# Kernel optimization log

Measured on AMD Instinct MI355X. Metric: run time of the kernel, lower is better.

The kernel has to match this reference:

```python
import jax, jax.numpy as jnp
import numpy as np

N = 100000
E = 1600000
DIN = 128
DOUT = 128
NUM_STEPS = 3


def setup_inputs() -> dict:
    key = jax.random.key(0)
    ks = jax.random.split(key, 12)
    stdv = 1.0 / np.sqrt(DOUT)
    xav = np.sqrt(6.0 / (2 * DOUT + DOUT))  # xavier_uniform for [DOUT, 2*DOUT]
    return {
        "input": jax.random.normal(ks[0], (N, DIN), dtype=jnp.float32),
        "edge_row": jax.random.randint(ks[1], (E,), 0, N, dtype=jnp.int32),
        "edge_col": jax.random.randint(ks[2], (E,), 0, N, dtype=jnp.int32),
        "edge_weight": jax.random.uniform(ks[3], (E,), dtype=jnp.float32),
        "weight": jax.random.uniform(ks[4], (DIN, DOUT), jnp.float32, -stdv, stdv),
        "bias": jax.random.uniform(ks[5], (DOUT,), jnp.float32, -stdv, stdv),
        "candidate_weight": jax.random.uniform(ks[6], (DOUT, DOUT), jnp.float32, -stdv, stdv),
        "ug_W": jax.random.uniform(ks[7], (DOUT, 2 * DOUT), jnp.float32, -xav, xav),
        "ug_b": jnp.zeros((DOUT,), jnp.float32),
        "rg_W": jax.random.uniform(ks[8], (DOUT, 2 * DOUT), jnp.float32, -xav, xav),
        "rg_b": jnp.zeros((DOUT,), jnp.float32),
    }


def reference(input, edge_row, edge_col, edge_weight, weight, bias,
              candidate_weight, ug_W, ug_b, rg_W, rg_b):
    n = input.shape[0]
    # h = input @ W + b
    h = input @ weight + bias
    for _ in range(NUM_STEPS):
        # spmm: m[dst] += w_e * h[src]
        msg = edge_weight[:, None] * h[edge_col]          # [E, DOUT]
        m = jax.ops.segment_sum(msg, edge_row, num_segments=n)  # [N, DOUT]
        g = jnp.concatenate([h, m], axis=1)               # [N, 2*DOUT]
        z = jax.nn.sigmoid(g @ ug_W.T + ug_b)
        r = jax.nn.sigmoid(g @ rg_W.T + rg_b)
        cand = jnp.tanh((r * h) @ candidate_weight)
        h = z * h + (1.0 - z) * cand
    return h
```

## Files before the change

kernel.cpp:

```cpp
#include <hip/hip_runtime.h>
#include <math.h>

#define NN 100000
#define EE 1600000
#define D 128
#define NBK 782
#define SBLK 98
#define EPB 16384
#define EMAX 2048
#define INITB 3125

typedef __attribute__((ext_vector_type(8))) short short8;
typedef __attribute__((ext_vector_type(4))) float floatx4;

static __device__ __forceinline__ unsigned short f2bf(float f) {
  unsigned int u = __builtin_bit_cast(unsigned int, f);
  u = (u + 0x7fff + ((u >> 16) & 1)) >> 16;
  return (unsigned short)u;
}
static __device__ __forceinline__ unsigned int pk2(float a, float b) {
  return (unsigned int)f2bf(a) | ((unsigned int)f2bf(b) << 16);
}
static __device__ __forceinline__ float bflo(unsigned int u) { return __builtin_bit_cast(float, u << 16); }
static __device__ __forceinline__ float bfhi(unsigned int u) { return __builtin_bit_cast(float, u & 0xffff0000u); }
static __device__ __forceinline__ float bf2f(unsigned short s) {
  return __builtin_bit_cast(float, (unsigned int)s << 16);
}
static __device__ __forceinline__ float sig_f(float x) { return 1.f / (1.f + __expf(-x)); }
static __device__ __forceinline__ float tanh_f(float x) {
  float e = __expf(2.f * x);
  return 1.f - 2.f / (e + 1.f);
}
static __device__ __forceinline__ void fma8(float* acc, float w, uint4 h) {
  acc[0] += w * bflo(h.x); acc[1] += w * bfhi(h.x);
  acc[2] += w * bflo(h.y); acc[3] += w * bfhi(h.y);
  acc[4] += w * bflo(h.z); acc[5] += w * bfhi(h.z);
  acc[6] += w * bflo(h.w); acc[7] += w * bfhi(h.w);
}

__global__ __launch_bounds__(1024) void countpack(const int* __restrict__ erow, int* __restrict__ cnt_pb,
                                                  const float* __restrict__ ugW, const float* __restrict__ rgW,
                                                  const float* __restrict__ CW, const float* __restrict__ W,
                                                  unsigned int* __restrict__ packZR,
                                                  unsigned int* __restrict__ packCW,
                                                  unsigned int* __restrict__ packW) {
  __shared__ int s[NBK];
  const int tid = threadIdx.x;
  if (blockIdx.x < SBLK) {
    for (int b = tid; b < NBK; b += 1024) s[b] = 0;
    __syncthreads();
    const int base = blockIdx.x * EPB;
#pragma unroll
    for (int i = 0; i < 16; ++i) {
      int idx = base + i * 1024 + tid;
      if (idx < EE) atomicAdd(&s[erow[idx] >> 7], 1);
    }
    __syncthreads();
    for (int b = tid; b < NBK; b += 1024) cnt_pb[blockIdx.x * NBK + b] = s[b];
  } else {
    int g = (blockIdx.x - SBLK) * 16 + (tid >> 6);
    int lane = tid & 63;
    if (g < 128) {
      int nt = g >> 3, ks = g & 7;
      int o = nt * 16 + (lane & 15);
      int c0 = ks * 32 + (lane >> 4) * 8;
      const float* src = (o < 128 ? ugW + (size_t)o * 256 : rgW + (size_t)(o - 128) * 256) + c0;
      float4 f0 = ((const float4*)src)[0];
      float4 f1 = ((const float4*)src)[1];
      uint4 out;
      out.x = pk2(f0.x, f0.y);
      out.y = pk2(f0.z, f0.w);
      out.z = pk2(f1.x, f1.y);
      out.w = pk2(f1.z, f1.w);
      ((uint4*)packZR)[g * 64 + lane] = out;
    } else if (g < 192) {
      const float* M = (g < 160) ? CW : W;
      unsigned int* dst = (g < 160) ? packCW : packW;
      int gg = (g < 160) ? (g - 128) : (g - 160);
      int nt = gg >> 2, ks = gg & 3;
      int n = nt * 16 + (lane & 15);
      int k0 = ks * 32 + (lane >> 4) * 8;
      unsigned short v[8];
#pragma unroll
      for (int j = 0; j < 8; ++j) v[j] = f2bf(M[(size_t)(k0 + j) * 128 + n]);
      uint4 out;
      out.x = (unsigned int)v[0] | ((unsigned int)v[1] << 16);
      out.y = (unsigned int)v[2] | ((unsigned int)v[3] << 16);
      out.z = (unsigned int)v[4] | ((unsigned int)v[5] << 16);
      out.w = (unsigned int)v[6] | ((unsigned int)v[7] << 16);
      ((uint4*)dst)[gg * 64 + lane] = out;
    }
  }
}

__global__ __launch_bounds__(1024) void b_off(const int* __restrict__ cnt_pb,
                                              int* __restrict__ bucket_off, int* __restrict__ bucket_cur) {
  __shared__ int s[1024];
  const int t = threadIdx.x;
  int v = 0;
  if (t < NBK) {
    for (int j = 0; j < SBLK; ++j) v += cnt_pb[j * NBK + t];
  }
  s[t] = v;
  __syncthreads();
  for (int d = 1; d < 1024; d <<= 1) {
    int x = (t >= d) ? s[t - d] : 0;
    __syncthreads();
    s[t] += x;
    __syncthreads();
  }
  int excl = s[t] - v;
  if (t < NBK) { bucket_off[t] = excl; bucket_cur[t] = excl; }
  if (t == NBK - 1) bucket_off[NBK] = excl + v;
}

__global__ __launch_bounds__(1024) void b_scatter(const int* __restrict__ erow, const int* __restrict__ ecol,
                                                  const float* __restrict__ ew, const int* __restrict__ cnt_pb,
                                                  int* __restrict__ bucket_cur, int2* __restrict__ arena) {
  __shared__ int cur[NBK];
  const int tid = threadIdx.x;
  for (int b = tid; b < NBK; b += 1024) {
    int c = cnt_pb[blockIdx.x * NBK + b];
    cur[b] = c ? atomicAdd(&bucket_cur[b], c) : 0;
  }
  __syncthreads();
  const int base = blockIdx.x * EPB;
#pragma unroll
  for (int i = 0; i < 16; ++i) {
    int idx = base + i * 1024 + tid;
    if (idx < EE) {
      int r = erow[idx];
      int pos = atomicAdd(&cur[r >> 7], 1);
      int2 v;
      v.x = ecol[idx] | ((r & 127) << 24);
      v.y = __builtin_bit_cast(int, ew[idx]);
      arena[pos] = v;
    }
  }
}

__global__ __launch_bounds__(256) void sortinit(
    const int* __restrict__ bucket_off, const int2* __restrict__ arena,
    int2* __restrict__ edata, int* __restrict__ row_start,
    const float* __restrict__ X, const short* __restrict__ packW, const float* __restrict__ bias,
    unsigned short* __restrict__ h_bf) {
  __shared__ __align__(16) char smem[32 * 136 * 2];
  const int tid = threadIdx.x;

  if (blockIdx.x < NBK) {
    int* rcnt = (int*)smem;
    int* rcur = (int*)(smem + 512);
    const int b = blockIdx.x;
    const int lo = bucket_off[b], hi = bucket_off[b + 1];

    if (tid < 128) rcnt[tid] = 0;
    __syncthreads();
    for (int i = lo + tid; i < hi; i += 256) atomicAdd(&rcnt[(arena[i].x >> 24) & 127], 1);
    __syncthreads();
    int myc = (tid < 128) ? rcnt[tid] : 0;
    for (int d = 1; d < 128; d <<= 1) {
      int v = (tid < 128 && tid >= d) ? rcnt[tid - d] : 0;
      __syncthreads();
      if (tid < 128) rcnt[tid] += v;
      __syncthreads();
    }
    if (tid < 128) {
      int excl = rcnt[tid] - myc;
      rcur[tid] = lo + excl;
      int gr = b * 128 + tid;
      if (gr < NN) row_start[gr] = lo + excl;
    }
    if (b == NBK - 1 && tid == 0) row_start[NN] = hi;
    __syncthreads();

    for (int i = lo + tid; i < hi; i += 256) {
      int2 v = arena[i];
      int rl = (v.x >> 24) & 127;
      int pos = atomicAdd(&rcur[rl], 1);
      int2 o;
      o.x = v.x & 0x00FFFFFF;
      o.y = v.y;
      edata[pos] = o;
    }
  } else {
    short* sX = (short*)smem;
    const int row0 = (blockIdx.x - NBK) * 32;

    {
      int r = tid >> 3, ch = tid & 7;
      const float4* px = (const float4*)(X + (size_t)(row0 + r) * D + ch * 16);
      float4 f0 = px[0], f1 = px[1], f2 = px[2], f3 = px[3];
      uint4 o0, o1;
      o0.x = pk2(f0.x, f0.y); o0.y = pk2(f0.z, f0.w);
      o0.z = pk2(f1.x, f1.y); o0.w = pk2(f1.z, f1.w);
      o1.x = pk2(f2.x, f2.y); o1.y = pk2(f2.z, f2.w);
      o1.z = pk2(f3.x, f3.y); o1.w = pk2(f3.z, f3.w);
      *(uint4*)(sX + r * 136 + ch * 16) = o0;
      *(uint4*)(sX + r * 136 + ch * 16 + 8) = o1;
    }
    __syncthreads();

    const int wave = tid >> 6, lane = tid & 63;
    const int quad = lane >> 4, l15 = lane & 15;
    const int mh = wave & 1, nh = wave >> 1;
    const int mrow = mh * 16 + l15;

    floatx4 acc[4];
    const floatx4 zero4 = {0.f, 0.f, 0.f, 0.f};
#pragma unroll
    for (int t = 0; t < 4; ++t) acc[t] = zero4;

    const short8* pW = (const short8*)packW;
#pragma unroll
    for (int ks = 0; ks < 4; ++ks) {
      short8 a = *(const short8*)(sX + mrow * 136 + ks * 32 + quad * 8);
#pragma unroll
      for (int t = 0; t < 4; ++t) {
        short8 b = pW[((nh * 4 + t) * 4 + ks) * 64 + lane];
        acc[t] = __builtin_amdgcn_mfma_f32_16x16x32_bf16(a, b, acc[t], 0, 0, 0);
      }
    }

    __syncthreads();
#pragma unroll
    for (int t = 0; t < 4; ++t) {
      int col = nh * 64 + t * 16 + l15;
      float bv = bias[col];
#pragma unroll
      for (int reg = 0; reg < 4; ++reg) {
        int row = mh * 16 + quad * 4 + reg;
        sX[row * 136 + col] = (short)f2bf(acc[t][reg] + bv);
      }
    }
    __syncthreads();
    for (int idx = tid; idx < 512; idx += 256) {
      int r = idx >> 4, ch = idx & 15;
      *(uint4*)(h_bf + (size_t)(row0 + r) * D + ch * 8) = *(uint4*)(sX + r * 136 + ch * 8);
    }
  }
}

__global__ __launch_bounds__(512, 8) void fused_step(
    const int* __restrict__ row_start, const int2* __restrict__ edata,
    const uint4* __restrict__ h4,
    const short* __restrict__ packZR, const short* __restrict__ packCW,
    const float* __restrict__ ugb, const float* __restrict__ rgb,
    unsigned short* __restrict__ h_bf_out, float* __restrict__ h_f32_out, int last) {
  __shared__ __align__(16) short sA[32 * 264];
  __shared__ __align__(16) char sU[EMAX * 8];
  int2* sE = (int2*)sU;
  short* sRH = (short*)sU;

  const int tid = threadIdx.x;
  const int row0 = blockIdx.x * 32;
  const int wave = tid >> 6, lane = tid & 63;
  const int sub = lane >> 4, li = lane & 15;

  {
    int r = tid >> 4, ch = tid & 15;
    *(uint4*)(sA + r * 264 + ch * 8) = h4[(size_t)(row0 + r) * 16 + ch];
  }

  const int myrow = row0 + wave * 4 + sub;
  const int rs0 = row_start[myrow];
  const int rs1 = row_start[myrow + 1];
  const int seg_lo = row_start[row0];
  const int seg_hi = row_start[row0 + 32];

  float acc[8];
#pragma unroll
  for (int j = 0; j < 8; ++j) acc[j] = 0.f;

  for (int clo = seg_lo; clo < seg_hi; clo += EMAX) {
    const int chi = min(clo + EMAX, seg_hi);
    for (int i = clo + tid; i < chi; i += 512) sE[i - clo] = edata[i];
    __syncthreads();

    int kb = max(rs0, clo) - clo;
    int ke = min(rs1, chi) - clo;
    for (; kb + 2 <= ke; kb += 2) {
      int2 e0 = sE[kb];
      int2 e1 = sE[kb + 1];
      uint4 h0 = h4[(size_t)e0.x * 16 + li];
      uint4 h1 = h4[(size_t)e1.x * 16 + li];
      fma8(acc, __builtin_bit_cast(float, e0.y), h0);
      fma8(acc, __builtin_bit_cast(float, e1.y), h1);
    }
    if (kb < ke) {
      int2 e0 = sE[kb];
      uint4 h0 = h4[(size_t)e0.x * 16 + li];
      fma8(acc, __builtin_bit_cast(float, e0.y), h0);
    }
    __syncthreads();
  }

  {
    uint4 o;
    o.x = pk2(acc[0], acc[1]);
    o.y = pk2(acc[2], acc[3]);
    o.z = pk2(acc[4], acc[5]);
    o.w = pk2(acc[6], acc[7]);
    *(uint4*)(sA + (wave * 4 + sub) * 264 + 128 + li * 8) = o;
  }
  __syncthreads();

  const int quad = lane >> 4, l15 = lane & 15;
  const int mh = wave >> 2, nh = wave & 3;
  const int mrow = mh * 16 + l15;

  floatx4 accZ[2], accR[2];
  const floatx4 zero4 = {0.f, 0.f, 0.f, 0.f};
#pragma unroll
  for (int t = 0; t < 2; ++t) { accZ[t] = zero4; accR[t] = zero4; }

  const short8* pB = (const short8*)packZR;
#pragma unroll
  for (int ks = 0; ks < 8; ++ks) {
    short8 a = *(const short8*)(sA + mrow * 264 + ks * 32 + quad * 8);
#pragma unroll
    for (int t = 0; t < 2; ++t) {
      short8 bz = pB[((nh * 2 + t) * 8 + ks) * 64 + lane];
      accZ[t] = __builtin_amdgcn_mfma_f32_16x16x32_bf16(a, bz, accZ[t], 0, 0, 0);
      short8 br = pB[((8 + nh * 2 + t) * 8 + ks) * 64 + lane];
      accR[t] = __builtin_amdgcn_mfma_f32_16x16x32_bf16(a, br, accR[t], 0, 0, 0);
    }
  }

#pragma unroll
  for (int t = 0; t < 2; ++t) {
    int col = nh * 32 + t * 16 + l15;
    float zb = ugb[col], rb = rgb[col];
#pragma unroll
    for (int reg = 0; reg < 4; ++reg) {
      int row = mh * 16 + quad * 4 + reg;
      float z = sig_f(accZ[t][reg] + zb);
      float rr = sig_f(accR[t][reg] + rb);
      float hv = bf2f((unsigned short)sA[row * 264 + col]);
      sRH[row * 136 + col] = (short)f2bf(rr * hv);
      accZ[t][reg] = z;
    }
  }
  __syncthreads();

  floatx4 acc2[2];
#pragma unroll
  for (int t = 0; t < 2; ++t) acc2[t] = zero4;

  const short8* pC = (const short8*)packCW;
#pragma unroll
  for (int ks = 0; ks < 4; ++ks) {
    short8 a = *(const short8*)(sRH + mrow * 136 + ks * 32 + quad * 8);
#pragma unroll
    for (int t = 0; t < 2; ++t) {
      short8 b = pC[((nh * 2 + t) * 4 + ks) * 64 + lane];
      acc2[t] = __builtin_amdgcn_mfma_f32_16x16x32_bf16(a, b, acc2[t], 0, 0, 0);
    }
  }

#pragma unroll
  for (int t = 0; t < 2; ++t) {
    int col = nh * 32 + t * 16 + l15;
#pragma unroll
    for (int reg = 0; reg < 4; ++reg) {
      int row = mh * 16 + quad * 4 + reg;
      float cand = tanh_f(acc2[t][reg]);
      float z = accZ[t][reg];
      float hold = bf2f((unsigned short)sA[row * 264 + col]);
      float hn = z * hold + (1.f - z) * cand;
      if (last) h_f32_out[(size_t)(row0 + row) * D + col] = hn;
      else sA[row * 264 + col] = (short)f2bf(hn);
    }
  }
  if (!last) {
    __syncthreads();
    int r = tid >> 4, ch = tid & 15;
    *(uint4*)(h_bf_out + (size_t)(row0 + r) * D + ch * 8) = *(uint4*)(sA + r * 264 + ch * 8);
  }
}

extern "C" void kernel_launch(void* const* d_in, const int* in_sizes, int n_in,
                              void* d_out, int out_size, void* d_ws, size_t ws_size,
                              hipStream_t stream) {
  const float* input = (const float*)d_in[0];
  const int* erow    = (const int*)d_in[1];
  const int* ecol    = (const int*)d_in[2];
  const float* ew    = (const float*)d_in[3];
  const float* W     = (const float*)d_in[4];
  const float* bias  = (const float*)d_in[5];
  const float* CW    = (const float*)d_in[6];
  const float* ugW   = (const float*)d_in[7];
  const float* ugb   = (const float*)d_in[8];
  const float* rgW   = (const float*)d_in[9];
  const float* rgb   = (const float*)d_in[10];

  float* h_out = (float*)d_out;

  char* ws = (char*)d_ws;
  unsigned short* hA = (unsigned short*)ws;   ws += (size_t)NN * D * 2;
  unsigned short* hB = (unsigned short*)ws;   ws += (size_t)NN * D * 2;
  unsigned int* packZR = (unsigned int*)ws;   ws += 16 * 8 * 64 * 16;
  unsigned int* packCW = (unsigned int*)ws;   ws += 8 * 4 * 64 * 16;
  unsigned int* packW  = (unsigned int*)ws;   ws += 8 * 4 * 64 * 16;
  int2* arena    = (int2*)ws;                 ws += (size_t)EE * sizeof(int2);
  int2* edata    = (int2*)ws;                 ws += (size_t)EE * sizeof(int2);
  int* cnt_pb    = (int*)ws;                  ws += (size_t)SBLK * NBK * sizeof(int);
  int* bucket_off= (int*)ws;                  ws += (NBK + 1) * sizeof(int);
  int* bucket_cur= (int*)ws;                  ws += NBK * sizeof(int);
  int* row_start = (int*)ws;                  ws += (NN + 1) * sizeof(int);

  countpack<<<SBLK + 12, 1024, 0, stream>>>(erow, cnt_pb, ugW, rgW, CW, W, packZR, packCW, packW);
  b_off<<<1, 1024, 0, stream>>>(cnt_pb, bucket_off, bucket_cur);
  b_scatter<<<SBLK, 1024, 0, stream>>>(erow, ecol, ew, cnt_pb, bucket_cur, arena);
  sortinit<<<NBK + INITB, 256, 0, stream>>>(bucket_off, arena, edata, row_start,
                                            input, (const short*)packW, bias, hA);

  fused_step<<<NN / 32, 512, 0, stream>>>(row_start, edata, (const uint4*)hA,
                                          (const short*)packZR, (const short*)packCW,
                                          ugb, rgb, hB, h_out, 0);
  fused_step<<<NN / 32, 512, 0, stream>>>(row_start, edata, (const uint4*)hB,
                                          (const short*)packZR, (const short*)packCW,
                                          ugb, rgb, hA, h_out, 0);
  fused_step<<<NN / 32, 512, 0, stream>>>(row_start, edata, (const uint4*)hA,
                                          (const short*)packZR, (const short*)packCW,
                                          ugb, rgb, hB, h_out, 1);
}
```

Baseline: 490.6 us.

## Replace global CSR sort with fixed-capacity row buckets sorted in-kernel

```diff
diff --git a/kernel.cpp b/kernel.cpp
--- a/kernel.cpp
+++ b/kernel.cpp
@@ -4,11 +4,10 @@
 #define NN 100000
 #define EE 1600000
 #define D 128
-#define NBK 782
+#define NBK 3125
 #define SBLK 98
 #define EPB 16384
-#define EMAX 2048
-#define INITB 3125
+#define CAP 1024
 
 typedef __attribute__((ext_vector_type(8))) short short8;
 typedef __attribute__((ext_vector_type(4))) float floatx4;
@@ -38,25 +37,43 @@
   acc[6] += w * bflo(h.w); acc[7] += w * bfhi(h.w);
 }
 
-__global__ __launch_bounds__(1024) void countpack(const int* __restrict__ erow, int* __restrict__ cnt_pb,
-                                                  const float* __restrict__ ugW, const float* __restrict__ rgW,
-                                                  const float* __restrict__ CW, const float* __restrict__ W,
-                                                  unsigned int* __restrict__ packZR,
-                                                  unsigned int* __restrict__ packCW,
-                                                  unsigned int* __restrict__ packW) {
-  __shared__ int s[NBK];
+__global__ __launch_bounds__(1024) void scatterpack(
+    const int* __restrict__ erow, const int* __restrict__ ecol, const float* __restrict__ ew,
+    int* __restrict__ bucket_len, int2* __restrict__ arena,
+    const float* __restrict__ ugW, const float* __restrict__ rgW,
+    const float* __restrict__ CW, const float* __restrict__ W,
+    unsigned int* __restrict__ packZR, unsigned int* __restrict__ packCW,
+    unsigned int* __restrict__ packW) {
+  __shared__ int cur[NBK];
   const int tid = threadIdx.x;
   if (blockIdx.x < SBLK) {
-    for (int b = tid; b < NBK; b += 1024) s[b] = 0;
+    for (int b = tid; b < NBK; b += 1024) cur[b] = 0;
     __syncthreads();
     const int base = blockIdx.x * EPB;
+    int r[16];
 #pragma unroll
     for (int i = 0; i < 16; ++i) {
       int idx = base + i * 1024 + tid;
-      if (idx < EE) atomicAdd(&s[erow[idx] >> 7], 1);
+      r[i] = (idx < EE) ? erow[idx] : -1;
+      if (r[i] >= 0) atomicAdd(&cur[r[i] >> 5], 1);
     }
     __syncthreads();
-    for (int b = tid; b < NBK; b += 1024) cnt_pb[blockIdx.x * NBK + b] = s[b];
+    for (int b = tid; b < NBK; b += 1024) {
+      int c = cur[b];
+      cur[b] = c ? (b * CAP + atomicAdd(&bucket_len[b], c)) : 0;
+    }
+    __syncthreads();
+#pragma unroll
+    for (int i = 0; i < 16; ++i) {
+      if (r[i] >= 0) {
+        int idx = base + i * 1024 + tid;
+        int pos = atomicAdd(&cur[r[i] >> 5], 1);
+        int2 v;
+        v.x = ecol[idx] | ((r[i] & 31) << 24);
+        v.y = __builtin_bit_cast(int, ew[idx]);
+        arena[pos] = v;
+      }
+    }
   } else {
     int g = (blockIdx.x - SBLK) * 16 + (tid >> 6);
     int lane = tid & 63;
@@ -93,166 +110,84 @@
   }
 }
 
-__global__ __launch_bounds__(1024) void b_off(const int* __restrict__ cnt_pb,
-                                              int* __restrict__ bucket_off, int* __restrict__ bucket_cur) {
-  __shared__ int s[1024];
-  const int t = threadIdx.x;
-  int v = 0;
-  if (t < NBK) {
-    for (int j = 0; j < SBLK; ++j) v += cnt_pb[j * NBK + t];
-  }
-  s[t] = v;
-  __syncthreads();
-  for (int d = 1; d < 1024; d <<= 1) {
-    int x = (t >= d) ? s[t - d] : 0;
-    __syncthreads();
-    s[t] += x;
-    __syncthreads();
-  }
-  int excl = s[t] - v;
-  if (t < NBK) { bucket_off[t] = excl; bucket_cur[t] = excl; }
-  if (t == NBK - 1) bucket_off[NBK] = excl + v;
-}
-
-__global__ __launch_bounds__(1024) void b_scatter(const int* __restrict__ erow, const int* __restrict__ ecol,
-                                                  const float* __restrict__ ew, const int* __restrict__ cnt_pb,
-                                                  int* __restrict__ bucket_cur, int2* __restrict__ arena) {
-  __shared__ int cur[NBK];
-  const int tid = threadIdx.x;
-  for (int b = tid; b < NBK; b += 1024) {
-    int c = cnt_pb[blockIdx.x * NBK + b];
-    cur[b] = c ? atomicAdd(&bucket_cur[b], c) : 0;
-  }
-  __syncthreads();
-  const int base = blockIdx.x * EPB;
-#pragma unroll
-  for (int i = 0; i < 16; ++i) {
-    int idx = base + i * 1024 + tid;
-    if (idx < EE) {
-      int r = erow[idx];
-      int pos = atomicAdd(&cur[r >> 7], 1);
-      int2 v;
-      v.x = ecol[idx] | ((r & 127) << 24);
-      v.y = __builtin_bit_cast(int, ew[idx]);
-      arena[pos] = v;
-    }
-  }
-}
-
-__global__ __launch_bounds__(256) void sortinit(
-    const int* __restrict__ bucket_off, const int2* __restrict__ arena,
-    int2* __restrict__ edata, int* __restrict__ row_start,
+__global__ __launch_bounds__(256) void init_mfma(
     const float* __restrict__ X, const short* __restrict__ packW, const float* __restrict__ bias,
     unsigned short* __restrict__ h_bf) {
-  __shared__ __align__(16) char smem[32 * 136 * 2];
+  __shared__ __align__(16) short sX[32 * 136];
   const int tid = threadIdx.x;
-
-  if (blockIdx.x < NBK) {
-    int* rcnt = (int*)smem;
-    int* rcur = (int*)(smem + 512);
-    const int b = blockIdx.x;
-    const int lo = bucket_off[b], hi = bucket_off[b + 1];
-
-    if (tid < 128) rcnt[tid] = 0;
-    __syncthreads();
-    for (int i = lo + tid; i < hi; i += 256) atomicAdd(&rcnt[(arena[i].x >> 24) & 127], 1);
-    __syncthreads();
-    int myc = (tid < 128) ? rcnt[tid] : 0;
-    for (int d = 1; d < 128; d <<= 1) {
-      int v = (tid < 128 && tid >= d) ? rcnt[tid - d] : 0;
-      __syncthreads();
-      if (tid < 128) rcnt[tid] += v;
-      __syncthreads();
-    }
-    if (tid < 128) {
-      int excl = rcnt[tid] - myc;
-      rcur[tid] = lo + excl;
-      int gr = b * 128 + tid;
-      if (gr < NN) row_start[gr] = lo + excl;
-    }
-    if (b == NBK - 1 && tid == 0) row_start[NN] = hi;
-    __syncthreads();
-
-    for (int i = lo + tid; i < hi; i += 256) {
-      int2 v = arena[i];
-      int rl = (v.x >> 24) & 127;
-      int pos = atomicAdd(&rcur[rl], 1);
-      int2 o;
-      o.x = v.x & 0x00FFFFFF;
-      o.y = v.y;
-      edata[pos] = o;
-    }
-  } else {
-    short* sX = (short*)smem;
-    const int row0 = (blockIdx.x - NBK) * 32;
-
-    {
-      int r = tid >> 3, ch = tid & 7;
-      const float4* px = (const float4*)(X + (size_t)(row0 + r) * D + ch * 16);
-      float4 f0 = px[0], f1 = px[1], f2 = px[2], f3 = px[3];
-      uint4 o0, o1;
-      o0.x = pk2(f0.x, f0.y); o0.y = pk2(f0.z, f0.w);
-      o0.z = pk2(f1.x, f1.y); o0.w = pk2(f1.z, f1.w);
-      o1.x = pk2(f2.x, f2.y); o1.y = pk2(f2.z, f2.w);
-      o1.z = pk2(f3.x, f3.y); o1.w = pk2(f3.z, f3.w);
-      *(uint4*)(sX + r * 136 + ch * 16) = o0;
-      *(uint4*)(sX + r * 136 + ch * 16 + 8) = o1;
-    }
-    __syncthreads();
-
-    const int wave = tid >> 6, lane = tid & 63;
-    const int quad = lane >> 4, l15 = lane & 15;
-    const int mh = wave & 1, nh = wave >> 1;
-    const int mrow = mh * 16 + l15;
-
-    floatx4 acc[4];
-    const floatx4 zero4 = {0.f, 0.f, 0.f, 0.f};
-#pragma unroll
-    for (int t = 0; t < 4; ++t) acc[t] = zero4;
-
-    const short8* pW = (const short8*)packW;
-#pragma unroll
-    for (int ks = 0; ks < 4; ++ks) {
-      short8 a = *(const short8*)(sX + mrow * 136 + ks * 32 + quad * 8);
-#pragma unroll
-      for (int t = 0; t < 4; ++t) {
-        short8 b = pW[((nh * 4 + t) * 4 + ks) * 64 + lane];
-        acc[t] = __builtin_amdgcn_mfma_f32_16x16x32_bf16(a, b, acc[t], 0, 0, 0);
-      }
-    }
-
-    __syncthreads();
+  const int row0 = blockIdx.x * 32;
+
+  {
+    int r = tid >> 3, ch = tid & 7;
+    const float4* px = (const float4*)(X + (size_t)(row0 + r) * D + ch * 16);
+    float4 f0 = px[0], f1 = px[1], f2 = px[2], f3 = px[3];
+    uint4 o0, o1;
+    o0.x = pk2(f0.x, f0.y); o0.y = pk2(f0.z, f0.w);
+    o0.z = pk2(f1.x, f1.y); o0.w = pk2(f1.z, f1.w);
+    o1.x = pk2(f2.x, f2.y); o1.y = pk2(f2.z, f2.w);
+    o1.z = pk2(f3.x, f3.y); o1.w = pk2(f3.z, f3.w);
+    *(uint4*)(sX + r * 136 + ch * 16) = o0;
+    *(uint4*)(sX + r * 136 + ch * 16 + 8) = o1;
+  }
+  __syncthreads();
+
+  const int wave = tid >> 6, lane = tid & 63;
+  const int quad = lane >> 4, l15 = lane & 15;
+  const int mh = wave & 1, nh = wave >> 1;
+  const int mrow = mh * 16 + l15;
+
+  floatx4 acc[4];
+  const floatx4 zero4 = {0.f, 0.f, 0.f, 0.f};
+#pragma unroll
+  for (int t = 0; t < 4; ++t) acc[t] = zero4;
+
+  const short8* pW = (const short8*)packW;
+#pragma unroll
+  for (int ks = 0; ks < 4; ++ks) {
+    short8 a = *(const short8*)(sX + mrow * 136 + ks * 32 + quad * 8);
 #pragma unroll
     for (int t = 0; t < 4; ++t) {
-      int col = nh * 64 + t * 16 + l15;
-      float bv = bias[col];
-#pragma unroll
-      for (int reg = 0; reg < 4; ++reg) {
-        int row = mh * 16 + quad * 4 + reg;
-        sX[row * 136 + col] = (short)f2bf(acc[t][reg] + bv);
-      }
-    }
-    __syncthreads();
-    for (int idx = tid; idx < 512; idx += 256) {
-      int r = idx >> 4, ch = idx & 15;
-      *(uint4*)(h_bf + (size_t)(row0 + r) * D + ch * 8) = *(uint4*)(sX + r * 136 + ch * 8);
-    }
+      short8 b = pW[((nh * 4 + t) * 4 + ks) * 64 + lane];
+      acc[t] = __builtin_amdgcn_mfma_f32_16x16x32_bf16(a, b, acc[t], 0, 0, 0);
+    }
+  }
+
+  __syncthreads();
+#pragma unroll
+  for (int t = 0; t < 4; ++t) {
+    int col = nh * 64 + t * 16 + l15;
+    float bv = bias[col];
+#pragma unroll
+    for (int reg = 0; reg < 4; ++reg) {
+      int row = mh * 16 + quad * 4 + reg;
+      sX[row * 136 + col] = (short)f2bf(acc[t][reg] + bv);
+    }
+  }
+  __syncthreads();
+  for (int idx = tid; idx < 512; idx += 256) {
+    int r = idx >> 4, ch = idx & 15;
+    *(uint4*)(h_bf + (size_t)(row0 + r) * D + ch * 8) = *(uint4*)(sX + r * 136 + ch * 8);
   }
 }
 
 __global__ __launch_bounds__(512, 8) void fused_step(
-    const int* __restrict__ row_start, const int2* __restrict__ edata,
+    const int* __restrict__ bucket_len, const int2* __restrict__ arena,
     const uint4* __restrict__ h4,
     const short* __restrict__ packZR, const short* __restrict__ packCW,
     const float* __restrict__ ugb, const float* __restrict__ rgb,
     unsigned short* __restrict__ h_bf_out, float* __restrict__ h_f32_out, int last) {
   __shared__ __align__(16) short sA[32 * 264];
-  __shared__ __align__(16) char sU[EMAX * 8];
-  int2* sE = (int2*)sU;
+  __shared__ __align__(16) char sU[8704];
+  __shared__ __align__(16) int2 sE2[CAP];
+  __shared__ int rcnt[32];
+  __shared__ int rstart[32];
+  __shared__ int rcur[32];
+  int2* sE_raw = (int2*)sU;
   short* sRH = (short*)sU;
 
   const int tid = threadIdx.x;
-  const int row0 = blockIdx.x * 32;
+  const int bid = blockIdx.x;
+  const int row0 = bid * 32;
   const int wave = tid >> 6, lane = tid & 63;
   const int sub = lane >> 4, li = lane & 15;
 
@@ -261,37 +196,52 @@
     *(uint4*)(sA + r * 264 + ch * 8) = h4[(size_t)(row0 + r) * 16 + ch];
   }
 
-  const int myrow = row0 + wave * 4 + sub;
-  const int rs0 = row_start[myrow];
-  const int rs1 = row_start[myrow + 1];
-  const int seg_lo = row_start[row0];
-  const int seg_hi = row_start[row0 + 32];
-
+  const int lo = bid * CAP;
+  int len = bucket_len[bid];
+  len = (len < CAP) ? len : CAP;
+
+  if (tid < 32) rcnt[tid] = 0;
+  for (int i = tid; i < len; i += 512) sE_raw[i] = arena[lo + i];
+  __syncthreads();
+  for (int i = tid; i < len; i += 512) atomicAdd(&rcnt[(sE_raw[i].x >> 24) & 31], 1);
+  __syncthreads();
+  if (tid < 64) {
+    int v = (tid < 32) ? rcnt[tid] : 0;
+    int inc = v;
+#pragma unroll
+    for (int d = 1; d < 32; d <<= 1) {
+      int u = __shfl_up(inc, d, 64);
+      if (tid >= d) inc += u;
+    }
+    if (tid < 32) { rstart[tid] = inc - v; rcur[tid] = inc - v; }
+  }
+  __syncthreads();
+  for (int i = tid; i < len; i += 512) {
+    int2 e = sE_raw[i];
+    int pos = atomicAdd(&rcur[(e.x >> 24) & 31], 1);
+    sE2[pos] = e;
+  }
+  __syncthreads();
+
+  const int rl = wave * 4 + sub;
   float acc[8];
 #pragma unroll
   for (int j = 0; j < 8; ++j) acc[j] = 0.f;
 
-  for (int clo = seg_lo; clo < seg_hi; clo += EMAX) {
-    const int chi = min(clo + EMAX, seg_hi);
-    for (int i = clo + tid; i < chi; i += 512) sE[i - clo] = edata[i];
-    __syncthreads();
-
-    int kb = max(rs0, clo) - clo;
-    int ke = min(rs1, chi) - clo;
-    for (; kb + 2 <= ke; kb += 2) {
-      int2 e0 = sE[kb];
-      int2 e1 = sE[kb + 1];
-      uint4 h0 = h4[(size_t)e0.x * 16 + li];
-      uint4 h1 = h4[(size_t)e1.x * 16 + li];
-      fma8(acc, __builtin_bit_cast(float, e0.y), h0);
-      fma8(acc, __builtin_bit_cast(float, e1.y), h1);
-    }
-    if (kb < ke) {
-      int2 e0 = sE[kb];
-      uint4 h0 = h4[(size_t)e0.x * 16 + li];
-      fma8(acc, __builtin_bit_cast(float, e0.y), h0);
-    }
-    __syncthreads();
+  int kb = rstart[rl];
+  int ke = kb + rcnt[rl];
+  for (; kb + 2 <= ke; kb += 2) {
+    int2 e0 = sE2[kb];
+    int2 e1 = sE2[kb + 1];
+    uint4 h0 = h4[(size_t)(e0.x & 0x00FFFFFF) * 16 + li];
+    uint4 h1 = h4[(size_t)(e1.x & 0x00FFFFFF) * 16 + li];
+    fma8(acc, __builtin_bit_cast(float, e0.y), h0);
+    fma8(acc, __builtin_bit_cast(float, e1.y), h1);
+  }
+  if (kb < ke) {
+    int2 e0 = sE2[kb];
+    uint4 h0 = h4[(size_t)(e0.x & 0x00FFFFFF) * 16 + li];
+    fma8(acc, __builtin_bit_cast(float, e0.y), h0);
   }
 
   {
@@ -401,26 +351,21 @@
   unsigned int* packZR = (unsigned int*)ws;   ws += 16 * 8 * 64 * 16;
   unsigned int* packCW = (unsigned int*)ws;   ws += 8 * 4 * 64 * 16;
   unsigned int* packW  = (unsigned int*)ws;   ws += 8 * 4 * 64 * 16;
-  int2* arena    = (int2*)ws;                 ws += (size_t)EE * sizeof(int2);
-  int2* edata    = (int2*)ws;                 ws += (size_t)EE * sizeof(int2);
-  int* cnt_pb    = (int*)ws;                  ws += (size_t)SBLK * NBK * sizeof(int);
-  int* bucket_off= (int*)ws;                  ws += (NBK + 1) * sizeof(int);
-  int* bucket_cur= (int*)ws;                  ws += NBK * sizeof(int);
-  int* row_start = (int*)ws;                  ws += (NN + 1) * sizeof(int);
-
-  countpack<<<SBLK + 12, 1024, 0, stream>>>(erow, cnt_pb, ugW, rgW, CW, W, packZR, packCW, packW);
-  b_off<<<1, 1024, 0, stream>>>(cnt_pb, bucket_off, bucket_cur);
-  b_scatter<<<SBLK, 1024, 0, stream>>>(erow, ecol, ew, cnt_pb, bucket_cur, arena);
-  sortinit<<<NBK + INITB, 256, 0, stream>>>(bucket_off, arena, edata, row_start,
-                                            input, (const short*)packW, bias, hA);
-
-  fused_step<<<NN / 32, 512, 0, stream>>>(row_start, edata, (const uint4*)hA,
-                                          (const short*)packZR, (const short*)packCW,
-                                          ugb, rgb, hB, h_out, 0);
-  fused_step<<<NN / 32, 512, 0, stream>>>(row_start, edata, (const uint4*)hB,
-                                          (const short*)packZR, (const short*)packCW,
-                                          ugb, rgb, hA, h_out, 0);
-  fused_step<<<NN / 32, 512, 0, stream>>>(row_start, edata, (const uint4*)hA,
-                                          (const short*)packZR, (const short*)packCW,
-                                          ugb, rgb, hB, h_out, 1);
-}
+  int2* arena    = (int2*)ws;                 ws += (size_t)NBK * CAP * sizeof(int2);
+  int* bucket_len= (int*)ws;                  ws += NBK * sizeof(int);
+
+  hipMemsetAsync(bucket_len, 0, NBK * sizeof(int), stream);
+  scatterpack<<<SBLK + 12, 1024, 0, stream>>>(erow, ecol, ew, bucket_len, arena,
+                                              ugW, rgW, CW, W, packZR, packCW, packW);
+  init_mfma<<<NN / 32, 256, 0, stream>>>(input, (const short*)packW, bias, hA);
+
+  fused_step<<<NBK, 512, 0, stream>>>(bucket_len, arena, (const uint4*)hA,
+                                      (const short*)packZR, (const short*)packCW,
+                                      ugb, rgb, hB, h_out, 0);
+  fused_step<<<NBK, 512, 0, stream>>>(bucket_len, arena, (const uint4*)hB,
+                                      (const short*)packZR, (const short*)packCW,
+                                      ugb, rgb, hA, h_out, 0);
+  fused_step<<<NBK, 512, 0, stream>>>(bucket_len, arena, (const uint4*)hA,
+                                      (const short*)packZR, (const short*)packCW,
+                                      ugb, rgb, hB, h_out, 1);
+}
```

After: 498.6 us. About the same (+1.6%).

## Merge preprocessing kernels into one cooperative kernel with grid syncs

Applied to the files above, without the earlier changes.

```diff
diff --git a/kernel.cpp b/kernel.cpp
--- a/kernel.cpp
+++ b/kernel.cpp
@@ -1,14 +1,19 @@
 #include <hip/hip_runtime.h>
+#include <hip/hip_cooperative_groups.h>
 #include <math.h>
+
+namespace cg = cooperative_groups;
 
 #define NN 100000
 #define EE 1600000
 #define D 128
 #define NBK 782
-#define SBLK 98
-#define EPB 16384
+#define GG 256
+#define TB 1024
+#define CNTB 244
+#define EPB1 6558
+#define EPB2 6250
 #define EMAX 2048
-#define INITB 3125
 
 typedef __attribute__((ext_vector_type(8))) short short8;
 typedef __attribute__((ext_vector_type(4))) float floatx4;
@@ -38,27 +43,32 @@
   acc[6] += w * bflo(h.w); acc[7] += w * bfhi(h.w);
 }
 
-__global__ __launch_bounds__(1024) void countpack(const int* __restrict__ erow, int* __restrict__ cnt_pb,
-                                                  const float* __restrict__ ugW, const float* __restrict__ rgW,
-                                                  const float* __restrict__ CW, const float* __restrict__ W,
-                                                  unsigned int* __restrict__ packZR,
-                                                  unsigned int* __restrict__ packCW,
-                                                  unsigned int* __restrict__ packW) {
-  __shared__ int s[NBK];
+__global__ __launch_bounds__(1024) void prep(
+    const int* __restrict__ erow, const int* __restrict__ ecol, const float* __restrict__ ew,
+    const float* __restrict__ ugW, const float* __restrict__ rgW,
+    const float* __restrict__ CW, const float* __restrict__ W,
+    const float* __restrict__ X, const float* __restrict__ bias,
+    unsigned int* __restrict__ packZR, unsigned int* __restrict__ packCW,
+    unsigned int* __restrict__ packW,
+    int* __restrict__ cnt_pb, int* __restrict__ bucket_off, int* __restrict__ bucket_cur,
+    int2* __restrict__ arena, int2* __restrict__ edata, int* __restrict__ row_start,
+    unsigned short* __restrict__ h_bf) {
+  cg::grid_group grid = cg::this_grid();
+  __shared__ __align__(16) char sm[34816];
   const int tid = threadIdx.x;
-  if (blockIdx.x < SBLK) {
-    for (int b = tid; b < NBK; b += 1024) s[b] = 0;
-    __syncthreads();
-    const int base = blockIdx.x * EPB;
-#pragma unroll
-    for (int i = 0; i < 16; ++i) {
-      int idx = base + i * 1024 + tid;
-      if (idx < EE) atomicAdd(&s[erow[idx] >> 7], 1);
-    }
-    __syncthreads();
-    for (int b = tid; b < NBK; b += 1024) cnt_pb[blockIdx.x * NBK + b] = s[b];
+  const int blk = blockIdx.x;
+
+  if (blk < CNTB) {
+    int* s = (int*)sm;
+    for (int b = tid; b < NBK; b += TB) s[b] = 0;
+    __syncthreads();
+    const int e0 = blk * EPB1;
+    const int e1 = min(e0 + EPB1, EE);
+    for (int i = e0 + tid; i < e1; i += TB) atomicAdd(&s[erow[i] >> 7], 1);
+    __syncthreads();
+    for (int b = tid; b < NBK; b += TB) cnt_pb[b * GG + blk] = s[b];
   } else {
-    int g = (blockIdx.x - SBLK) * 16 + (tid >> 6);
+    int g = (blk - CNTB) * 16 + (tid >> 6);
     int lane = tid & 63;
     if (g < 128) {
       int nt = g >> 3, ks = g & 7;
@@ -91,151 +101,147 @@
       ((uint4*)dst)[gg * 64 + lane] = out;
     }
   }
-}
-
-__global__ __launch_bounds__(1024) void b_off(const int* __restrict__ cnt_pb,
-                                              int* __restrict__ bucket_off, int* __restrict__ bucket_cur) {
-  __shared__ int s[1024];
-  const int t = threadIdx.x;
-  int v = 0;
-  if (t < NBK) {
-    for (int j = 0; j < SBLK; ++j) v += cnt_pb[j * NBK + t];
-  }
-  s[t] = v;
-  __syncthreads();
-  for (int d = 1; d < 1024; d <<= 1) {
-    int x = (t >= d) ? s[t - d] : 0;
-    __syncthreads();
-    s[t] += x;
-    __syncthreads();
-  }
-  int excl = s[t] - v;
-  if (t < NBK) { bucket_off[t] = excl; bucket_cur[t] = excl; }
-  if (t == NBK - 1) bucket_off[NBK] = excl + v;
-}
-
-__global__ __launch_bounds__(1024) void b_scatter(const int* __restrict__ erow, const int* __restrict__ ecol,
-                                                  const float* __restrict__ ew, const int* __restrict__ cnt_pb,
-                                                  int* __restrict__ bucket_cur, int2* __restrict__ arena) {
-  __shared__ int cur[NBK];
-  const int tid = threadIdx.x;
-  for (int b = tid; b < NBK; b += 1024) {
-    int c = cnt_pb[blockIdx.x * NBK + b];
-    cur[b] = c ? atomicAdd(&bucket_cur[b], c) : 0;
-  }
-  __syncthreads();
-  const int base = blockIdx.x * EPB;
-#pragma unroll
-  for (int i = 0; i < 16; ++i) {
-    int idx = base + i * 1024 + tid;
-    if (idx < EE) {
-      int r = erow[idx];
+  grid.sync();
+
+  if (blk == 0) {
+    int* s2 = (int*)sm;
+    int v = 0;
+    if (tid < NBK) {
+      const int* row = cnt_pb + (size_t)tid * GG;
+      for (int j = 0; j < CNTB; ++j) v += row[j];
+    }
+    s2[tid] = v;
+    __syncthreads();
+    for (int d = 1; d < TB; d <<= 1) {
+      int x = (tid >= d) ? s2[tid - d] : 0;
+      __syncthreads();
+      s2[tid] += x;
+      __syncthreads();
+    }
+    int excl = s2[tid] - v;
+    if (tid < NBK) { bucket_off[tid] = excl; bucket_cur[tid] = excl; }
+    if (tid == NBK - 1) bucket_off[NBK] = excl + v;
+  } else {
+    short* sX = (short*)(sm + (tid >> 8) * 8704);
+    const int t = tid & 255;
+    const int w4 = t >> 6, lane = tid & 63;
+    const int quad = lane >> 4, l15 = lane & 15;
+    const int mh = w4 & 1, nh = w4 >> 1;
+    const int mrow = mh * 16 + l15;
+    const short8* pW = (const short8*)packW;
+    const floatx4 zero4 = {0.f, 0.f, 0.f, 0.f};
+    for (int p = 0; p < 4; ++p) {
+      int u = (blk - 1) + 255 * p;
+      int tile = u * 4 + (tid >> 8);
+      bool valid = (u < 1024) && (tile < NN / 32);
+      int row0 = valid ? tile * 32 : 0;
+      {
+        int r = t >> 3, ch = t & 7;
+        const float4* px = (const float4*)(X + (size_t)(row0 + r) * D + ch * 16);
+        float4 f0 = px[0], f1 = px[1], f2 = px[2], f3 = px[3];
+        uint4 o0, o1;
+        o0.x = pk2(f0.x, f0.y); o0.y = pk2(f0.z, f0.w);
+        o0.z = pk2(f1.x, f1.y); o0.w = pk2(f1.z, f1.w);
+        o1.x = pk2(f2.x, f2.y); o1.y = pk2(f2.z, f2.w);
+        o1.z = pk2(f3.x, f3.y); o1.w = pk2(f3.z, f3.w);
+        *(uint4*)(sX + r * 136 + ch * 16) = o0;
+        *(uint4*)(sX + r * 136 + ch * 16 + 8) = o1;
+      }
+      __syncthreads();
+      floatx4 acc[4];
+#pragma unroll
+      for (int tt = 0; tt < 4; ++tt) acc[tt] = zero4;
+#pragma unroll
+      for (int ks = 0; ks < 4; ++ks) {
+        short8 a = *(const short8*)(sX + mrow * 136 + ks * 32 + quad * 8);
+#pragma unroll
+        for (int tt = 0; tt < 4; ++tt) {
+          short8 b = pW[((nh * 4 + tt) * 4 + ks) * 64 + lane];
+          acc[tt] = __builtin_amdgcn_mfma_f32_16x16x32_bf16(a, b, acc[tt], 0, 0, 0);
+        }
+      }
+      __syncthreads();
+#pragma unroll
+      for (int tt = 0; tt < 4; ++tt) {
+        int col = nh * 64 + tt * 16 + l15;
+        float bv = bias[col];
+#pragma unroll
+        for (int reg = 0; reg < 4; ++reg) {
+          int row = mh * 16 + quad * 4 + reg;
+          sX[row * 136 + col] = (short)f2bf(acc[tt][reg] + bv);
+        }
+      }
+      __syncthreads();
+      if (valid) {
+        int r = t >> 3, ch0 = (t & 7) * 2;
+        *(uint4*)(h_bf + (size_t)(row0 + r) * D + ch0 * 8) = *(uint4*)(sX + r * 136 + ch0 * 8);
+        *(uint4*)(h_bf + (size_t)(row0 + r) * D + ch0 * 8 + 8) = *(uint4*)(sX + r * 136 + ch0 * 8 + 8);
+      }
+      __syncthreads();
+    }
+  }
+  grid.sync();
+
+  {
+    int* cur = (int*)sm;
+    for (int b = tid; b < NBK; b += TB) cur[b] = 0;
+    __syncthreads();
+    const int e0 = blk * EPB2;
+    const int e1 = e0 + EPB2;
+    for (int i = e0 + tid; i < e1; i += TB) atomicAdd(&cur[erow[i] >> 7], 1);
+    __syncthreads();
+    for (int b = tid; b < NBK; b += TB) {
+      int c = cur[b];
+      cur[b] = c ? atomicAdd(&bucket_cur[b], c) : 0;
+    }
+    __syncthreads();
+    for (int i = e0 + tid; i < e1; i += TB) {
+      int r = erow[i];
       int pos = atomicAdd(&cur[r >> 7], 1);
       int2 v;
-      v.x = ecol[idx] | ((r & 127) << 24);
-      v.y = __builtin_bit_cast(int, ew[idx]);
+      v.x = ecol[i] | ((r & 127) << 24);
+      v.y = __builtin_bit_cast(int, ew[i]);
       arena[pos] = v;
     }
   }
-}
-
-__global__ __launch_bounds__(256) void sortinit(
-    const int* __restrict__ bucket_off, const int2* __restrict__ arena,
-    int2* __restrict__ edata, int* __restrict__ row_start,
-    const float* __restrict__ X, const short* __restrict__ packW, const float* __restrict__ bias,
-    unsigned short* __restrict__ h_bf) {
-  __shared__ __align__(16) char smem[32 * 136 * 2];
-  const int tid = threadIdx.x;
-
-  if (blockIdx.x < NBK) {
-    int* rcnt = (int*)smem;
-    int* rcur = (int*)(smem + 512);
-    const int b = blockIdx.x;
-    const int lo = bucket_off[b], hi = bucket_off[b + 1];
-
-    if (tid < 128) rcnt[tid] = 0;
-    __syncthreads();
-    for (int i = lo + tid; i < hi; i += 256) atomicAdd(&rcnt[(arena[i].x >> 24) & 127], 1);
-    __syncthreads();
-    int myc = (tid < 128) ? rcnt[tid] : 0;
-    for (int d = 1; d < 128; d <<= 1) {
-      int v = (tid < 128 && tid >= d) ? rcnt[tid - d] : 0;
-      __syncthreads();
-      if (tid < 128) rcnt[tid] += v;
-      __syncthreads();
-    }
-    if (tid < 128) {
-      int excl = rcnt[tid] - myc;
-      rcur[tid] = lo + excl;
-      int gr = b * 128 + tid;
-      if (gr < NN) row_start[gr] = lo + excl;
-    }
-    if (b == NBK - 1 && tid == 0) row_start[NN] = hi;
-    __syncthreads();
-
-    for (int i = lo + tid; i < hi; i += 256) {
-      int2 v = arena[i];
-      int rl = (v.x >> 24) & 127;
-      int pos = atomicAdd(&rcur[rl], 1);
-      int2 o;
-      o.x = v.x & 0x00FFFFFF;
-      o.y = v.y;
-      edata[pos] = o;
-    }
-  } else {
-    short* sX = (short*)smem;
-    const int row0 = (blockIdx.x - NBK) * 32;
-
-    {
-      int r = tid >> 3, ch = tid & 7;
-      const float4* px = (const float4*)(X + (size_t)(row0 + r) * D + ch * 16);
-      float4 f0 = px[0], f1 = px[1], f2 = px[2], f3 = px[3];
-      uint4 o0, o1;
-      o0.x = pk2(f0.x, f0.y); o0.y = pk2(f0.z, f0.w);
-      o0.z = pk2(f1.x, f1.y); o0.w = pk2(f1.z, f1.w);
-      o1.x = pk2(f2.x, f2.y); o1.y = pk2(f2.z, f2.w);
-      o1.z = pk2(f3.x, f3.y); o1.w = pk2(f3.z, f3.w);
-      *(uint4*)(sX + r * 136 + ch * 16) = o0;
-      *(uint4*)(sX + r * 136 + ch * 16 + 8) = o1;
-    }
-    __syncthreads();
-
-    const int wave = tid >> 6, lane = tid & 63;
-    const int quad = lane >> 4, l15 = lane & 15;
-    const int mh = wave & 1, nh = wave >> 1;
-    const int mrow = mh * 16 + l15;
-
-    floatx4 acc[4];
-    const floatx4 zero4 = {0.f, 0.f, 0.f, 0.f};
-#pragma unroll
-    for (int t = 0; t < 4; ++t) acc[t] = zero4;
-
-    const short8* pW = (const short8*)packW;
-#pragma unroll
-    for (int ks = 0; ks < 4; ++ks) {
-      short8 a = *(const short8*)(sX + mrow * 136 + ks * 32 + quad * 8);
-#pragma unroll
-      for (int t = 0; t < 4; ++t) {
-        short8 b = pW[((nh * 4 + t) * 4 + ks) * 64 + lane];
-        acc[t] = __builtin_amdgcn_mfma_f32_16x16x32_bf16(a, b, acc[t], 0, 0, 0);
-      }
-    }
-
-    __syncthreads();
-#pragma unroll
-    for (int t = 0; t < 4; ++t) {
-      int col = nh * 64 + t * 16 + l15;
-      float bv = bias[col];
-#pragma unroll
-      for (int reg = 0; reg < 4; ++reg) {
-        int row = mh * 16 + quad * 4 + reg;
-        sX[row * 136 + col] = (short)f2bf(acc[t][reg] + bv);
-      }
-    }
-    __syncthreads();
-    for (int idx = tid; idx < 512; idx += 256) {
-      int r = idx >> 4, ch = idx & 15;
-      *(uint4*)(h_bf + (size_t)(row0 + r) * D + ch * 8) = *(uint4*)(sX + r * 136 + ch * 8);
+  grid.sync();
+
+  {
+    int* rcnt = (int*)sm;
+    int* rcur = rcnt + 128;
+    for (int p = 0; p < 4; ++p) {
+      int b = blk + GG * p;
+      int lo = 0, hi = 0;
+      if (b < NBK) { lo = bucket_off[b]; hi = bucket_off[b + 1]; }
+      if (tid < 128) rcnt[tid] = 0;
+      __syncthreads();
+      for (int i = lo + tid; i < hi; i += TB) atomicAdd(&rcnt[(arena[i].x >> 24) & 127], 1);
+      __syncthreads();
+      int myc = (tid < 128) ? rcnt[tid] : 0;
+      for (int d = 1; d < 128; d <<= 1) {
+        int v = (tid < 128 && tid >= d) ? rcnt[tid - d] : 0;
+        __syncthreads();
+        if (tid < 128) rcnt[tid] += v;
+        __syncthreads();
+      }
+      if (b < NBK && tid < 128) {
+        int excl = rcnt[tid] - myc;
+        rcur[tid] = lo + excl;
+        int gr = b * 128 + tid;
+        if (gr < NN) row_start[gr] = lo + excl;
+      }
+      if (b == NBK - 1 && tid == 0) row_start[NN] = hi;
+      __syncthreads();
+      for (int i = lo + tid; i < hi; i += TB) {
+        int2 v = arena[i];
+        int rl = (v.x >> 24) & 127;
+        int pos = atomicAdd(&rcur[rl], 1);
+        int2 o;
+        o.x = v.x & 0x00FFFFFF;
+        o.y = v.y;
+        edata[pos] = o;
+      }
+      __syncthreads();
     }
   }
 }
@@ -403,16 +409,20 @@
   unsigned int* packW  = (unsigned int*)ws;   ws += 8 * 4 * 64 * 16;
   int2* arena    = (int2*)ws;                 ws += (size_t)EE * sizeof(int2);
   int2* edata    = (int2*)ws;                 ws += (size_t)EE * sizeof(int2);
-  int* cnt_pb    = (int*)ws;                  ws += (size_t)SBLK * NBK * sizeof(int);
+  int* cnt_pb    = (int*)ws;                  ws += (size_t)NBK * GG * sizeof(int);
   int* bucket_off= (int*)ws;                  ws += (NBK + 1) * sizeof(int);
   int* bucket_cur= (int*)ws;                  ws += NBK * sizeof(int);
   int* row_start = (int*)ws;                  ws += (NN + 1) * sizeof(int);
 
-  countpack<<<SBLK + 12, 1024, 0, stream>>>(erow, cnt_pb, ugW, rgW, CW, W, packZR, packCW, packW);
-  b_off<<<1, 1024, 0, stream>>>(cnt_pb, bucket_off, bucket_cur);
-  b_scatter<<<SBLK, 1024, 0, stream>>>(erow, ecol, ew, cnt_pb, bucket_cur, arena);
-  sortinit<<<NBK + INITB, 256, 0, stream>>>(bucket_off, arena, edata, row_start,
-                                            input, (const short*)packW, bias, hA);
+  void* args[] = {
+    (void*)&erow, (void*)&ecol, (void*)&ew,
+    (void*)&ugW, (void*)&rgW, (void*)&CW, (void*)&W,
+    (void*)&input, (void*)&bias,
+    (void*)&packZR, (void*)&packCW, (void*)&packW,
+    (void*)&cnt_pb, (void*)&bucket_off, (void*)&bucket_cur,
+    (void*)&arena, (void*)&edata, (void*)&row_start, (void*)&hA
+  };
+  hipLaunchCooperativeKernel((const void*)prep, dim3(GG), dim3(TB), args, 0, stream);
 
   fused_step<<<NN / 32, 512, 0, stream>>>(row_start, edata, (const uint4*)hA,
                                           (const short*)packZR, (const short*)packCW,
```

After: 621.0 us. +26.6%, slower.
